# Optimization experiments

Measured on AMD Instinct MI355X. Metric: run time of the kernel, lower is better.

The kernel has to match this reference:

```python
import jax, jax.numpy as jnp
import numpy as np

K = 3
STRIDE = 1
PAD = 1


def _conv2d(x, w, b):
    y = jax.lax.conv_general_dilated(
        x, w, window_strides=(STRIDE, STRIDE),
        padding=[(PAD, PAD), (PAD, PAD)],
        dimension_numbers=("NCHW", "OIHW", "NCHW"))
    return y + b[None, :, None, None]


def _bilinear_sample(xb, py, px):
    # xb: [C, H, W]; py, px: [K2, Ho, Wo] float sample coords
    C, H, W = xb.shape
    y0 = jnp.floor(py)
    x0 = jnp.floor(px)
    ay = py - y0  # frac weights
    ax = px - x0
    out = jnp.zeros((C,) + py.shape, dtype=xb.dtype)
    corners = [
        (y0, x0, (1.0 - ay) * (1.0 - ax)),
        (y0, x0 + 1.0, (1.0 - ay) * ax),
        (y0 + 1.0, x0, ay * (1.0 - ax)),
        (y0 + 1.0, x0 + 1.0, ay * ax),
    ]
    for yc, xc, wgt in corners:
        valid = (yc >= 0) & (yc < H) & (xc >= 0) & (xc < W)
        yi = jnp.clip(yc, 0, H - 1).astype(jnp.int32)
        xi = jnp.clip(xc, 0, W - 1).astype(jnp.int32)
        g = xb[:, yi, xi]  # [C, K2, Ho, Wo]
        out = out + g * (wgt * valid.astype(xb.dtype))[None]
    return out


def _deform_forward(x, weight, bias, p_weight, p_bias):
    B, Cin, H, W = x.shape
    Cout = weight.shape[0]
    K2 = K * K
    # offset / mask prediction conv
    pout = _conv2d(x, p_weight, p_bias)  # [B, 3*K2, Ho, Wo]
    o1, o2, m = jnp.split(pout, 3, axis=1)
    offset = jnp.concatenate([o1, o2], axis=1)  # [B, 2*K2, Ho, Wo]
    mask = jax.nn.sigmoid(m)  # [B, K2, Ho, Wo]
    Ho, Wo = mask.shape[2], mask.shape[3]
    # torchvision layout: channel 2k = dy_k, 2k+1 = dx_k
    off = offset.reshape(B, K2, 2, Ho, Wo)
    dy, dx = off[:, :, 0], off[:, :, 1]  # [B, K2, Ho, Wo]
    ki = (jnp.arange(K2) // K).astype(x.dtype)  # kernel row
    kj = (jnp.arange(K2) % K).astype(x.dtype)   # kernel col
    base_y = jnp.arange(Ho, dtype=x.dtype) * STRIDE - PAD  # [Ho]
    base_x = jnp.arange(Wo, dtype=x.dtype) * STRIDE - PAD  # [Wo]
    py = base_y[None, None, :, None] + ki[None, :, None, None] + dy
    px = base_x[None, None, None, :] + kj[None, :, None, None] + dx
    sampled = jax.vmap(_bilinear_sample)(x, py, px)  # [B, Cin, K2, Ho, Wo]
    sampled = sampled * mask[:, None]
    w = weight.reshape(Cout, Cin, K2)
    out = jnp.einsum('bckhw,ock->bohw', sampled, w) + bias[None, :, None, None]
    return out


def setup_inputs() -> dict:
    key = jax.random.key(0)
    k1, k2, k3 = jax.random.split(key, 3)
    B, Cin, Cout, H, W = 4, 256, 256, 64, 64
    x = jax.random.normal(k1, (B, Cin, H, W), dtype=jnp.float32)
    fan_in = Cin * K * K
    weight = jax.random.normal(k2, (Cout, Cin, K, K), dtype=jnp.float32) / np.sqrt(fan_in)
    bias = jnp.zeros((Cout,), dtype=jnp.float32)
    # small random offset/mask predictor (zero-init in the original; randomized
    # here so the deformable sampling path is exercised)
    p_weight = jax.random.normal(k3, (3 * K * K, Cin, K, K), dtype=jnp.float32) * 0.02
    p_bias = jnp.zeros((3 * K * K,), dtype=jnp.float32)
    return {"x": x, "weight": weight, "bias": bias, "p_weight": p_weight, "p_bias": p_bias}


def reference(x, weight, bias, p_weight, p_bias):
    return _deform_forward(x, weight, bias, p_weight, p_bias)
```

## Files before the change

kernel.cpp:

```cpp
#include <hip/hip_runtime.h>
#include <stdint.h>


#define CIN 256
#define COUT 256
#define HWS 4096
#define MTOT 16384
#define KTOT 2304
#define SPLITK 8

typedef __attribute__((ext_vector_type(8))) short bf16x8;
typedef __attribute__((ext_vector_type(4))) float f32x4;

__device__ __forceinline__ unsigned short f2bf(float f) {
  unsigned int u = __float_as_uint(f);
  unsigned int r = (u + 0x7fffu + ((u >> 16) & 1u)) >> 16;
  return (unsigned short)r;
}
__device__ __forceinline__ float bf2f(unsigned short u) {
  return __uint_as_float(((unsigned int)u) << 16);
}

__device__ __forceinline__ void gload_lds16(const void* g, void* l) {
  __builtin_amdgcn_global_load_lds((const __attribute__((address_space(1))) void*)g,
                                   (__attribute__((address_space(3))) void*)l, 16, 0, 0);
}

__global__ __launch_bounds__(256) void prep_and_transpose(const float* __restrict__ x,
                                                          const float* __restrict__ w,
                                                          const float* __restrict__ pw,
                                                          unsigned short* __restrict__ xt,
                                                          unsigned short* __restrict__ WB,
                                                          unsigned short* __restrict__ PWs,
                                                          unsigned short* __restrict__ zerop) {
  __shared__ float tile[32][33];
  int bid = blockIdx.x;
  if (bid < 4096) {
    int b = bid >> 10;
    int rest = bid & 1023;
    int hw0 = (rest & 127) * 32;
    int c0 = ((rest >> 7) & 7) * 32;
    int tx = threadIdx.x & 31, ty = threadIdx.x >> 5;
    for (int i = ty; i < 32; i += 8)
      tile[i][tx] = x[(size_t)(b * CIN + c0 + i) * HWS + hw0 + tx];
    __syncthreads();
    for (int r = ty; r < 32; r += 8)
      xt[(size_t)(b * HWS + hw0 + r) * CIN + c0 + tx] = f2bf(tile[tx][r]);
  } else {
    int idx = (bid - 4096) * 256 + threadIdx.x;
    if (idx < 512)
      *(uint4*)(zerop + idx * 8) = make_uint4(0, 0, 0, 0);
    if (idx < KTOT * COUT) {
      int f = idx;
      int e = f & 7;
      int row = (f >> 3) & 15;
      int quad = (f >> 7) & 3;
      int j = (f >> 9) & 15;
      int t = f >> 13;
      int kk = t * 32 + quad * 8 + e;
      int o = j * 16 + row;
      int k = kk >> 8, c = kk & 255;
      WB[f] = f2bf(w[o * KTOT + c * 9 + k]);
    } else {
      int f2 = idx - KTOT * COUT;
      int t_ = f2 & 7;
      int rest = f2 >> 3;
      int j = rest & 31;
      int kk = (rest >> 5) * 8 + t_;
      int k = kk >> 8, c = kk & 255;
      float v = (j < 27) ? pw[j * KTOT + c * 9 + k] : 0.0f;
      PWs[f2] = f2bf(v);
    }
  }
}

__global__ __launch_bounds__(256) void offset_conv_sk(const unsigned short* __restrict__ xt,
                                                      const unsigned short* __restrict__ PWs,
                                                      const unsigned short* __restrict__ zerop,
                                                      float* __restrict__ Pbuf) {
  __shared__ unsigned short Al[64 * 32];
  __shared__ unsigned short Bl[1024];
  int tid = threadIdx.x;
  int lane = tid & 63, wv = tid >> 6;
  int mt = (blockIdx.x & 7) * 32 + (blockIdx.x >> 3);
  int m0 = mt * 64;
  int s = blockIdx.y;
  int b = m0 >> 12;
  int hw0 = m0 & 4095;
  f32x4 acc[2] = {};

  for (int tt = 0; tt < 72 / SPLITK; ++tt) {
    int t = s * (72 / SPLITK) + tt;
    int k = t >> 3, c0 = (t & 7) * 32;
    int dyk = k / 3 - 1;
    int dxk = k % 3 - 1;
    __syncthreads();
    if (tid < 128)
      gload_lds16(PWs + (size_t)t * 1024 + tid * 8, &Bl[tid * 8]);
    {
      int r = tid >> 2;
      int hw = hw0 + r;
      int h = hw >> 6, wwp = hw & 63;
      int y = h + dyk, xx = wwp + dxk;
      bool valid = ((unsigned)y < 64u) && ((unsigned)xx < 64u);
      const unsigned short* src = valid
          ? xt + ((size_t)((b << 12) + (y << 6) + xx) << 8) + c0 + (tid & 3) * 8
          : zerop;
      gload_lds16(src, &Al[tid * 8]);
    }
    __syncthreads();
    int row = lane & 15, quad = lane >> 4;
    bf16x8 af = *(const bf16x8*)&Al[(wv * 16 + row) * 32 + quad * 8];
    for (int j = 0; j < 2; ++j) {
      bf16x8 bfr = *(const bf16x8*)&Bl[(quad * 32 + j * 16 + row) * 8];
      acc[j] = __builtin_amdgcn_mfma_f32_16x16x32_bf16(af, bfr, acc[j], 0, 0, 0);
    }
  }

  int row = lane & 15, quad = lane >> 4;
  for (int j = 0; j < 2; ++j) {
    int n = j * 16 + row;
    for (int r_ = 0; r_ < 4; ++r_) {
      int m = m0 + wv * 16 + quad * 4 + r_;
      Pbuf[((size_t)s * MTOT + m) * 32 + n] = acc[j][r_];
    }
  }
}

__global__ __launch_bounds__(256) void sample9(const unsigned short* __restrict__ xt,
                                               const float* __restrict__ Pbuf,
                                               const float* __restrict__ p_bias,
                                               unsigned short* __restrict__ A) {
  __shared__ int4 dI[4][9];
  __shared__ float4 dW[4][9];
  int tid = threadIdx.x;
  int reg = blockIdx.x & 7;
  int mb = reg * 2048 + (blockIdx.x >> 3) * 4;

  if (tid < 36) {
    int lm = tid / 9, k = tid - lm * 9;
    int m = mb + lm;
    float dy = p_bias[2 * k];
    float dx = p_bias[2 * k + 1];
    float mv = p_bias[18 + k];
#pragma unroll
    for (int s = 0; s < SPLITK; ++s) {
      const float* p = Pbuf + ((size_t)s * MTOT + m) * 32;
      dy += p[2 * k];
      dx += p[2 * k + 1];
      mv += p[18 + k];
    }
    float mk = 1.0f / (1.0f + __expf(-mv));

    int hw = m & 4095, h = hw >> 6, ww = hw & 63;
    float py = (float)(h - 1 + k / 3) + dy;
    float px = (float)(ww - 1 + k % 3) + dx;
    float y0f = floorf(py), x0f = floorf(px);
    float ay = py - y0f, ax = px - x0f;
    int y0 = (int)y0f, x0 = (int)x0f;

    float w00 = (1.f - ay) * (1.f - ax) * mk;
    float w01 = (1.f - ay) * ax * mk;
    float w10 = ay * (1.f - ax) * mk;
    float w11 = ay * ax * mk;

    float vy0 = ((unsigned)y0 < 64u) ? 1.f : 0.f;
    float vy1 = ((unsigned)(y0 + 1) < 64u) ? 1.f : 0.f;
    float vx0 = ((unsigned)x0 < 64u) ? 1.f : 0.f;
    float vx1 = ((unsigned)(x0 + 1) < 64u) ? 1.f : 0.f;
    w00 *= vy0 * vx0; w01 *= vy0 * vx1; w10 *= vy1 * vx0; w11 *= vy1 * vx1;

    int yc0 = min(max(y0, 0), 63), yc1 = min(max(y0 + 1, 0), 63);
    int xc0 = min(max(x0, 0), 63), xc1 = min(max(x0 + 1, 0), 63);

    dI[lm][k] = make_int4((yc0 * 64 + xc0) * 256, (yc0 * 64 + xc1) * 256,
                          (yc1 * 64 + xc0) * 256, (yc1 * 64 + xc1) * 256);
    dW[lm][k] = make_float4(w00, w01, w10, w11);
  }
  __syncthreads();

  int wv = tid >> 6, lane = tid & 63;
  int m = mb + wv;
  int b = m >> 12;
  const unsigned short* xtb = xt + (((size_t)b << 12) << 8);
  unsigned short* abase = A + (((size_t)(m >> 4) * 72 + (lane >> 3)) * 16 + (m & 15)) * 32
                            + ((lane >> 1) & 3) * 8 + (lane & 1) * 4;

#pragma unroll
  for (int k = 0; k < 9; ++k) {
    int4 o4 = dI[wv][k];
    float4 w4 = dW[wv][k];
    ushort4 t00 = *(const ushort4*)(xtb + o4.x + 4 * lane);
    ushort4 t01 = *(const ushort4*)(xtb + o4.y + 4 * lane);
    ushort4 t10 = *(const ushort4*)(xtb + o4.z + 4 * lane);
    ushort4 t11 = *(const ushort4*)(xtb + o4.w + 4 * lane);
    float r0 = w4.x * bf2f(t00.x) + w4.y * bf2f(t01.x) + w4.z * bf2f(t10.x) + w4.w * bf2f(t11.x);
    float r1 = w4.x * bf2f(t00.y) + w4.y * bf2f(t01.y) + w4.z * bf2f(t10.y) + w4.w * bf2f(t11.y);
    float r2 = w4.x * bf2f(t00.z) + w4.y * bf2f(t01.z) + w4.z * bf2f(t10.z) + w4.w * bf2f(t11.z);
    float r3 = w4.x * bf2f(t00.w) + w4.y * bf2f(t01.w) + w4.z * bf2f(t10.w) + w4.w * bf2f(t11.w);
    ushort4 o;
    o.x = f2bf(r0); o.y = f2bf(r1); o.z = f2bf(r2); o.w = f2bf(r3);
    *(ushort4*)(abase + (size_t)k * 8 * 512) = o;
  }
}

#define LOADSET(SA0, SA1, SB0, SB1, SB2, SB3, TT)                         \
  {                                                                       \
    const unsigned short* a0_ = ap0 + (size_t)(TT) * 512;                 \
    const unsigned short* a1_ = ap1 + (size_t)(TT) * 512;                 \
    const unsigned short* bt_ = bp + (size_t)(TT) * 8192;                 \
    SA0 = *(const bf16x8*)(a0_);                                          \
    SA1 = *(const bf16x8*)(a1_);                                          \
    SB0 = *(const bf16x8*)(bt_);                                          \
    SB1 = *(const bf16x8*)(bt_ + 512);                                    \
    SB2 = *(const bf16x8*)(bt_ + 1024);                                   \
    SB3 = *(const bf16x8*)(bt_ + 1536);                                   \
  }

#define COMPUTESET(SA0, SA1, SB0, SB1, SB2, SB3)                                        \
  acc[0][0] = __builtin_amdgcn_mfma_f32_16x16x32_bf16(SA0, SB0, acc[0][0], 0, 0, 0);    \
  acc[0][1] = __builtin_amdgcn_mfma_f32_16x16x32_bf16(SA0, SB1, acc[0][1], 0, 0, 0);    \
  acc[0][2] = __builtin_amdgcn_mfma_f32_16x16x32_bf16(SA0, SB2, acc[0][2], 0, 0, 0);    \
  acc[0][3] = __builtin_amdgcn_mfma_f32_16x16x32_bf16(SA0, SB3, acc[0][3], 0, 0, 0);    \
  acc[1][0] = __builtin_amdgcn_mfma_f32_16x16x32_bf16(SA1, SB0, acc[1][0], 0, 0, 0);    \
  acc[1][1] = __builtin_amdgcn_mfma_f32_16x16x32_bf16(SA1, SB1, acc[1][1], 0, 0, 0);    \
  acc[1][2] = __builtin_amdgcn_mfma_f32_16x16x32_bf16(SA1, SB2, acc[1][2], 0, 0, 0);    \
  acc[1][3] = __builtin_amdgcn_mfma_f32_16x16x32_bf16(SA1, SB3, acc[1][3], 0, 0, 0);

__global__ __launch_bounds__(256) void main_gemm(const unsigned short* __restrict__ A2,
                                                 const unsigned short* __restrict__ WB,
                                                 const float* __restrict__ bias,
                                                 float* __restrict__ out) {
  int tid = threadIdx.x;
  int lane = tid & 63, wv = tid >> 6;
  int bid = blockIdx.x;
  int xcd = bid & 7;
  int wgrp = bid >> 3;
  int mt = xcd * 16 + (wgrp >> 2);
  int nb = wgrp & 3;
  int m0 = mt * 128;
  int n0 = nb * 64;
  int wm = wv * 32;
  int row = lane & 15, quad = lane >> 4;
  f32x4 acc[2][4] = {};

  int mb0 = (m0 + wm) >> 4;
  const unsigned short* ap0 = A2 + (size_t)mb0 * 72 * 512 + row * 32 + quad * 8;
  const unsigned short* ap1 = ap0 + (size_t)72 * 512;
  const unsigned short* bp = WB + (size_t)(nb * 4) * 512 + quad * 128 + row * 8;

  bf16x8 s0a0, s0a1, s0b0, s0b1, s0b2, s0b3;
  bf16x8 s1a0, s1a1, s1b0, s1b1, s1b2, s1b3;
  bf16x8 s2a0, s2a1, s2b0, s2b1, s2b2, s2b3;
  bf16x8 s3a0, s3a1, s3b0, s3b1, s3b2, s3b3;

  LOADSET(s0a0, s0a1, s0b0, s0b1, s0b2, s0b3, 0)
  LOADSET(s1a0, s1a1, s1b0, s1b1, s1b2, s1b3, 1)
  LOADSET(s2a0, s2a1, s2b0, s2b1, s2b2, s2b3, 2)
  LOADSET(s3a0, s3a1, s3b0, s3b1, s3b2, s3b3, 3)

#pragma unroll 1
  for (int t = 0; t < 68; t += 4) {
    COMPUTESET(s0a0, s0a1, s0b0, s0b1, s0b2, s0b3)
    LOADSET(s0a0, s0a1, s0b0, s0b1, s0b2, s0b3, t + 4)
    COMPUTESET(s1a0, s1a1, s1b0, s1b1, s1b2, s1b3)
    LOADSET(s1a0, s1a1, s1b0, s1b1, s1b2, s1b3, t + 5)
    COMPUTESET(s2a0, s2a1, s2b0, s2b1, s2b2, s2b3)
    LOADSET(s2a0, s2a1, s2b0, s2b1, s2b2, s2b3, t + 6)
    COMPUTESET(s3a0, s3a1, s3b0, s3b1, s3b2, s3b3)
    LOADSET(s3a0, s3a1, s3b0, s3b1, s3b2, s3b3, t + 7)
  }
  COMPUTESET(s0a0, s0a1, s0b0, s0b1, s0b2, s0b3)
  COMPUTESET(s1a0, s1a1, s1b0, s1b1, s1b2, s1b3)
  COMPUTESET(s2a0, s2a1, s2b0, s2b1, s2b2, s2b3)
  COMPUTESET(s3a0, s3a1, s3b0, s3b1, s3b2, s3b3)

  int b = m0 >> 12, hw0 = m0 & 4095;
#pragma unroll
  for (int j = 0; j < 4; ++j) {
    int o = n0 + j * 16 + row;
    float bo = bias[o];
#pragma unroll
    for (int i = 0; i < 2; ++i) {
      int hw = hw0 + wm + i * 16 + quad * 4;
      float4 v;
      v.x = acc[i][j][0] + bo;
      v.y = acc[i][j][1] + bo;
      v.z = acc[i][j][2] + bo;
      v.w = acc[i][j][3] + bo;
      *(float4*)(out + (((size_t)(b * COUT + o)) << 12) + hw) = v;
    }
  }
}

extern "C" void kernel_launch(void* const* d_in, const int* in_sizes, int n_in,
                              void* d_out, int out_size, void* d_ws, size_t ws_size,
                              hipStream_t stream) {
  const float* x        = (const float*)d_in[0];
  const float* weight   = (const float*)d_in[1];
  const float* bias     = (const float*)d_in[2];
  const float* p_weight = (const float*)d_in[3];
  const float* p_bias   = (const float*)d_in[4];
  float* out = (float*)d_out;
  char* ws = (char*)d_ws;

  const size_t OFF_XT   = 0;
  const size_t OFF_WB   = OFF_XT + 8388608;
  const size_t OFF_PW   = OFF_WB + 1179648;
  const size_t OFF_P    = OFF_PW + 147456;
  const size_t OFF_ZP   = OFF_P + 16777216;
  const size_t OFF_A    = OFF_ZP + 8192;

  unsigned short* xt    = (unsigned short*)(ws + OFF_XT);
  unsigned short* WB    = (unsigned short*)(ws + OFF_WB);
  unsigned short* PWs   = (unsigned short*)(ws + OFF_PW);
  float* Pbuf           = (float*)(ws + OFF_P);
  unsigned short* zerop = (unsigned short*)(ws + OFF_ZP);
  unsigned short* Amat  = (unsigned short*)(ws + OFF_A);

  prep_and_transpose<<<4096 + 2592, 256, 0, stream>>>(x, weight, p_weight, xt, WB, PWs, zerop);
  offset_conv_sk<<<dim3(MTOT / 64, SPLITK), 256, 0, stream>>>(xt, PWs, zerop, Pbuf);
  sample9<<<MTOT / 4, 256, 0, stream>>>(xt, Pbuf, p_bias, Amat);
  main_gemm<<<512, 256, 0, stream>>>(Amat, WB, bias, out);
}
```

Measured before the change: 150.9 us.

## Fuse bilinear sampling into main GEMM, replacing materialized im2col matrix with index table

The sampling kernel that wrote a bf16 im2col matrix to global memory is split: a small kernel now precomputes per-(pixel, tap) corner offsets and weights. The GEMM kernel then gathers the four corners, interpolates into double-buffered LDS A tiles, and runs MFMA on them while prefetching the next K-slice. This removes the write and re-read of the large sampled matrix. In exchange the GEMM uses 64x256 tiles with only 256 blocks, a barrier every K step, and gather latency inside the main loop.

```diff
diff --git a/kernel.cpp b/kernel.cpp
--- a/kernel.cpp
+++ b/kernel.cpp
@@ -127,162 +127,183 @@
   }
 }
 
-__global__ __launch_bounds__(256) void sample9(const unsigned short* __restrict__ xt,
-                                               const float* __restrict__ Pbuf,
-                                               const float* __restrict__ p_bias,
-                                               unsigned short* __restrict__ A) {
-  __shared__ int4 dI[4][9];
-  __shared__ float4 dW[4][9];
-  int tid = threadIdx.x;
-  int reg = blockIdx.x & 7;
-  int mb = reg * 2048 + (blockIdx.x >> 3) * 4;
-
-  if (tid < 36) {
-    int lm = tid / 9, k = tid - lm * 9;
-    int m = mb + lm;
-    float dy = p_bias[2 * k];
-    float dx = p_bias[2 * k + 1];
-    float mv = p_bias[18 + k];
+__global__ __launch_bounds__(256) void index_prep(const float* __restrict__ Pbuf,
+                                                  const float* __restrict__ p_bias,
+                                                  int4* __restrict__ DIW) {
+  int gid = blockIdx.x * 256 + threadIdx.x;
+  int m = gid / 9;
+  int k = gid - m * 9;
+
+  float dy = p_bias[2 * k];
+  float dx = p_bias[2 * k + 1];
+  float mv = p_bias[18 + k];
 #pragma unroll
-    for (int s = 0; s < SPLITK; ++s) {
-      const float* p = Pbuf + ((size_t)s * MTOT + m) * 32;
-      dy += p[2 * k];
-      dx += p[2 * k + 1];
-      mv += p[18 + k];
-    }
-    float mk = 1.0f / (1.0f + __expf(-mv));
-
-    int hw = m & 4095, h = hw >> 6, ww = hw & 63;
-    float py = (float)(h - 1 + k / 3) + dy;
-    float px = (float)(ww - 1 + k % 3) + dx;
-    float y0f = floorf(py), x0f = floorf(px);
-    float ay = py - y0f, ax = px - x0f;
-    int y0 = (int)y0f, x0 = (int)x0f;
-
-    float w00 = (1.f - ay) * (1.f - ax) * mk;
-    float w01 = (1.f - ay) * ax * mk;
-    float w10 = ay * (1.f - ax) * mk;
-    float w11 = ay * ax * mk;
-
-    float vy0 = ((unsigned)y0 < 64u) ? 1.f : 0.f;
-    float vy1 = ((unsigned)(y0 + 1) < 64u) ? 1.f : 0.f;
-    float vx0 = ((unsigned)x0 < 64u) ? 1.f : 0.f;
-    float vx1 = ((unsigned)(x0 + 1) < 64u) ? 1.f : 0.f;
-    w00 *= vy0 * vx0; w01 *= vy0 * vx1; w10 *= vy1 * vx0; w11 *= vy1 * vx1;
-
-    int yc0 = min(max(y0, 0), 63), yc1 = min(max(y0 + 1, 0), 63);
-    int xc0 = min(max(x0, 0), 63), xc1 = min(max(x0 + 1, 0), 63);
-
-    dI[lm][k] = make_int4((yc0 * 64 + xc0) * 256, (yc0 * 64 + xc1) * 256,
-                          (yc1 * 64 + xc0) * 256, (yc1 * 64 + xc1) * 256);
-    dW[lm][k] = make_float4(w00, w01, w10, w11);
-  }
-  __syncthreads();
-
-  int wv = tid >> 6, lane = tid & 63;
-  int m = mb + wv;
-  int b = m >> 12;
-  const unsigned short* xtb = xt + (((size_t)b << 12) << 8);
-  unsigned short* abase = A + (((size_t)(m >> 4) * 72 + (lane >> 3)) * 16 + (m & 15)) * 32
-                            + ((lane >> 1) & 3) * 8 + (lane & 1) * 4;
-
+  for (int s = 0; s < SPLITK; ++s) {
+    const float* p = Pbuf + ((size_t)s * MTOT + m) * 32;
+    dy += p[2 * k];
+    dx += p[2 * k + 1];
+    mv += p[18 + k];
+  }
+  float mk = 1.0f / (1.0f + __expf(-mv));
+
+  int hw = m & 4095, h = hw >> 6, ww = hw & 63;
+  float py = (float)(h - 1 + k / 3) + dy;
+  float px = (float)(ww - 1 + k % 3) + dx;
+  float y0f = floorf(py), x0f = floorf(px);
+  float ay = py - y0f, ax = px - x0f;
+  int y0 = (int)y0f, x0 = (int)x0f;
+
+  float w00 = (1.f - ay) * (1.f - ax) * mk;
+  float w01 = (1.f - ay) * ax * mk;
+  float w10 = ay * (1.f - ax) * mk;
+  float w11 = ay * ax * mk;
+
+  float vy0 = ((unsigned)y0 < 64u) ? 1.f : 0.f;
+  float vy1 = ((unsigned)(y0 + 1) < 64u) ? 1.f : 0.f;
+  float vx0 = ((unsigned)x0 < 64u) ? 1.f : 0.f;
+  float vx1 = ((unsigned)(x0 + 1) < 64u) ? 1.f : 0.f;
+  w00 *= vy0 * vx0; w01 *= vy0 * vx1; w10 *= vy1 * vx0; w11 *= vy1 * vx1;
+
+  int yc0 = min(max(y0, 0), 63), yc1 = min(max(y0 + 1, 0), 63);
+  int xc0 = min(max(x0, 0), 63), xc1 = min(max(x0 + 1, 0), 63);
+
+  DIW[(size_t)gid * 2] = make_int4((yc0 * 64 + xc0) * 256, (yc0 * 64 + xc1) * 256,
+                                   (yc1 * 64 + xc0) * 256, (yc1 * 64 + xc1) * 256);
+  float4 w4 = make_float4(w00, w01, w10, w11);
+  ((float4*)DIW)[(size_t)gid * 2 + 1] = w4;
+}
+
+__device__ __forceinline__ void bilin8(const bf16x8 g00, const bf16x8 g01,
+                                       const bf16x8 g10, const bf16x8 g11,
+                                       const float4 w4, unsigned short* dst) {
+  bf16x8 o8;
 #pragma unroll
-  for (int k = 0; k < 9; ++k) {
-    int4 o4 = dI[wv][k];
-    float4 w4 = dW[wv][k];
-    ushort4 t00 = *(const ushort4*)(xtb + o4.x + 4 * lane);
-    ushort4 t01 = *(const ushort4*)(xtb + o4.y + 4 * lane);
-    ushort4 t10 = *(const ushort4*)(xtb + o4.z + 4 * lane);
-    ushort4 t11 = *(const ushort4*)(xtb + o4.w + 4 * lane);
-    float r0 = w4.x * bf2f(t00.x) + w4.y * bf2f(t01.x) + w4.z * bf2f(t10.x) + w4.w * bf2f(t11.x);
-    float r1 = w4.x * bf2f(t00.y) + w4.y * bf2f(t01.y) + w4.z * bf2f(t10.y) + w4.w * bf2f(t11.y);
-    float r2 = w4.x * bf2f(t00.z) + w4.y * bf2f(t01.z) + w4.z * bf2f(t10.z) + w4.w * bf2f(t11.z);
-    float r3 = w4.x * bf2f(t00.w) + w4.y * bf2f(t01.w) + w4.z * bf2f(t10.w) + w4.w * bf2f(t11.w);
-    ushort4 o;
-    o.x = f2bf(r0); o.y = f2bf(r1); o.z = f2bf(r2); o.w = f2bf(r3);
-    *(ushort4*)(abase + (size_t)k * 8 * 512) = o;
-  }
-}
-
-#define LOADSET(SA0, SA1, SB0, SB1, SB2, SB3, TT)                         \
-  {                                                                       \
-    const unsigned short* a0_ = ap0 + (size_t)(TT) * 512;                 \
-    const unsigned short* a1_ = ap1 + (size_t)(TT) * 512;                 \
-    const unsigned short* bt_ = bp + (size_t)(TT) * 8192;                 \
-    SA0 = *(const bf16x8*)(a0_);                                          \
-    SA1 = *(const bf16x8*)(a1_);                                          \
-    SB0 = *(const bf16x8*)(bt_);                                          \
-    SB1 = *(const bf16x8*)(bt_ + 512);                                    \
-    SB2 = *(const bf16x8*)(bt_ + 1024);                                   \
-    SB3 = *(const bf16x8*)(bt_ + 1536);                                   \
-  }
-
-#define COMPUTESET(SA0, SA1, SB0, SB1, SB2, SB3)                                        \
-  acc[0][0] = __builtin_amdgcn_mfma_f32_16x16x32_bf16(SA0, SB0, acc[0][0], 0, 0, 0);    \
-  acc[0][1] = __builtin_amdgcn_mfma_f32_16x16x32_bf16(SA0, SB1, acc[0][1], 0, 0, 0);    \
-  acc[0][2] = __builtin_amdgcn_mfma_f32_16x16x32_bf16(SA0, SB2, acc[0][2], 0, 0, 0);    \
-  acc[0][3] = __builtin_amdgcn_mfma_f32_16x16x32_bf16(SA0, SB3, acc[0][3], 0, 0, 0);    \
-  acc[1][0] = __builtin_amdgcn_mfma_f32_16x16x32_bf16(SA1, SB0, acc[1][0], 0, 0, 0);    \
-  acc[1][1] = __builtin_amdgcn_mfma_f32_16x16x32_bf16(SA1, SB1, acc[1][1], 0, 0, 0);    \
-  acc[1][2] = __builtin_amdgcn_mfma_f32_16x16x32_bf16(SA1, SB2, acc[1][2], 0, 0, 0);    \
-  acc[1][3] = __builtin_amdgcn_mfma_f32_16x16x32_bf16(SA1, SB3, acc[1][3], 0, 0, 0);
-
-__global__ __launch_bounds__(256) void main_gemm(const unsigned short* __restrict__ A2,
-                                                 const unsigned short* __restrict__ WB,
-                                                 const float* __restrict__ bias,
-                                                 float* __restrict__ out) {
+  for (int e = 0; e < 8; ++e) {
+    float v = w4.x * bf2f((unsigned short)g00[e]) + w4.y * bf2f((unsigned short)g01[e]) +
+              w4.z * bf2f((unsigned short)g10[e]) + w4.w * bf2f((unsigned short)g11[e]);
+    o8[e] = (short)f2bf(v);
+  }
+  *(bf16x8*)dst = o8;
+}
+
+#define MFMA16(A0, A1, A2_, A3, B0, B1, B2, B3)                                          \
+  acc[0][0] = __builtin_amdgcn_mfma_f32_16x16x32_bf16(A0, B0, acc[0][0], 0, 0, 0);       \
+  acc[0][1] = __builtin_amdgcn_mfma_f32_16x16x32_bf16(A0, B1, acc[0][1], 0, 0, 0);       \
+  acc[0][2] = __builtin_amdgcn_mfma_f32_16x16x32_bf16(A0, B2, acc[0][2], 0, 0, 0);       \
+  acc[0][3] = __builtin_amdgcn_mfma_f32_16x16x32_bf16(A0, B3, acc[0][3], 0, 0, 0);       \
+  acc[1][0] = __builtin_amdgcn_mfma_f32_16x16x32_bf16(A1, B0, acc[1][0], 0, 0, 0);       \
+  acc[1][1] = __builtin_amdgcn_mfma_f32_16x16x32_bf16(A1, B1, acc[1][1], 0, 0, 0);       \
+  acc[1][2] = __builtin_amdgcn_mfma_f32_16x16x32_bf16(A1, B2, acc[1][2], 0, 0, 0);       \
+  acc[1][3] = __builtin_amdgcn_mfma_f32_16x16x32_bf16(A1, B3, acc[1][3], 0, 0, 0);       \
+  acc[2][0] = __builtin_amdgcn_mfma_f32_16x16x32_bf16(A2_, B0, acc[2][0], 0, 0, 0);      \
+  acc[2][1] = __builtin_amdgcn_mfma_f32_16x16x32_bf16(A2_, B1, acc[2][1], 0, 0, 0);      \
+  acc[2][2] = __builtin_amdgcn_mfma_f32_16x16x32_bf16(A2_, B2, acc[2][2], 0, 0, 0);      \
+  acc[2][3] = __builtin_amdgcn_mfma_f32_16x16x32_bf16(A2_, B3, acc[2][3], 0, 0, 0);      \
+  acc[3][0] = __builtin_amdgcn_mfma_f32_16x16x32_bf16(A3, B0, acc[3][0], 0, 0, 0);       \
+  acc[3][1] = __builtin_amdgcn_mfma_f32_16x16x32_bf16(A3, B1, acc[3][1], 0, 0, 0);       \
+  acc[3][2] = __builtin_amdgcn_mfma_f32_16x16x32_bf16(A3, B2, acc[3][2], 0, 0, 0);       \
+  acc[3][3] = __builtin_amdgcn_mfma_f32_16x16x32_bf16(A3, B3, acc[3][3], 0, 0, 0);
+
+#define FITER(T, PAR, BC0, BC1, BC2, BC3, BN0, BN1, BN2, BN3)                            \
+  {                                                                                      \
+    if ((T) <= 69) {                                                                     \
+      if ((((T) + 2) & 7) == 0) dI4 = Tbl[r][((T) + 2) >> 3][0];                         \
+      int cq = (((T) + 2) & 7) * 32 + qo;                                                \
+      g00 = *(const bf16x8*)(xtb + dI4.x + cq);                                          \
+      g01 = *(const bf16x8*)(xtb + dI4.y + cq);                                          \
+      g10 = *(const bf16x8*)(xtb + dI4.z + cq);                                          \
+      g11 = *(const bf16x8*)(xtb + dI4.w + cq);                                          \
+    }                                                                                    \
+    if ((T) <= 70) {                                                                     \
+      const unsigned short* bt_ = bpb + (size_t)((T) + 1) * 8192;                        \
+      BN0 = *(const bf16x8*)(bt_);                                                       \
+      BN1 = *(const bf16x8*)(bt_ + 512);                                                 \
+      BN2 = *(const bf16x8*)(bt_ + 1024);                                                \
+      BN3 = *(const bf16x8*)(bt_ + 1536);                                                \
+    }                                                                                    \
+    afr0 = *(const bf16x8*)&As[PAR][row][quad * 8];                                      \
+    afr1 = *(const bf16x8*)&As[PAR][16 + row][quad * 8];                                 \
+    afr2 = *(const bf16x8*)&As[PAR][32 + row][quad * 8];                                 \
+    afr3 = *(const bf16x8*)&As[PAR][48 + row][quad * 8];                                 \
+    if ((T) <= 70) {                                                                     \
+      if ((((T) + 1) & 7) == 0) dW4 = *(float4*)&Tbl[r][((T) + 1) >> 3][1];              \
+      bilin8(gp0, gp1, gp2, gp3, dW4, &As[PAR ^ 1][r][qo]);                              \
+    }                                                                                    \
+    MFMA16(afr0, afr1, afr2, afr3, BC0, BC1, BC2, BC3)                                   \
+    __syncthreads();                                                                     \
+  }
+
+__global__ __launch_bounds__(256, 1) void fused_gemm(const unsigned short* __restrict__ xt,
+                                                     const int4* __restrict__ DIW,
+                                                     const unsigned short* __restrict__ WB,
+                                                     const float* __restrict__ bias,
+                                                     float* __restrict__ out) {
+  __shared__ unsigned short As[2][64][40];
+  __shared__ int4 Tbl[64][9][2];
+
   int tid = threadIdx.x;
   int lane = tid & 63, wv = tid >> 6;
-  int bid = blockIdx.x;
-  int xcd = bid & 7;
-  int wgrp = bid >> 3;
-  int mt = xcd * 16 + (wgrp >> 2);
-  int nb = wgrp & 3;
-  int m0 = mt * 128;
-  int n0 = nb * 64;
-  int wm = wv * 32;
+  int mt = (blockIdx.x & 7) * 32 + (blockIdx.x >> 3);
+  int mb = mt * 64;
+  int b = mb >> 12;
+  int hw0 = mb & 4095;
+  const unsigned short* xtb = xt + ((size_t)b << 20);
+
+  {
+    const int4* src = DIW + (size_t)mb * 18;
+    int4* dst = (int4*)Tbl;
+    for (int i = tid; i < 1152; i += 256)
+      gload_lds16(src + i, dst + i);
+  }
+  __syncthreads();
+
+  int r = tid >> 2;
+  int qo = (tid & 3) * 8;
+
+  int4 dI4 = Tbl[r][0][0];
+  float4 dW4 = *(float4*)&Tbl[r][0][1];
+
   int row = lane & 15, quad = lane >> 4;
-  f32x4 acc[2][4] = {};
-
-  int mb0 = (m0 + wm) >> 4;
-  const unsigned short* ap0 = A2 + (size_t)mb0 * 72 * 512 + row * 32 + quad * 8;
-  const unsigned short* ap1 = ap0 + (size_t)72 * 512;
-  const unsigned short* bp = WB + (size_t)(nb * 4) * 512 + quad * 128 + row * 8;
-
-  bf16x8 s0a0, s0a1, s0b0, s0b1, s0b2, s0b3;
-  bf16x8 s1a0, s1a1, s1b0, s1b1, s1b2, s1b3;
-  bf16x8 s2a0, s2a1, s2b0, s2b1, s2b2, s2b3;
-  bf16x8 s3a0, s3a1, s3b0, s3b1, s3b2, s3b3;
-
-  LOADSET(s0a0, s0a1, s0b0, s0b1, s0b2, s0b3, 0)
-  LOADSET(s1a0, s1a1, s1b0, s1b1, s1b2, s1b3, 1)
-  LOADSET(s2a0, s2a1, s2b0, s2b1, s2b2, s2b3, 2)
-  LOADSET(s3a0, s3a1, s3b0, s3b1, s3b2, s3b3, 3)
+  const unsigned short* bpb = WB + (size_t)wv * 4 * 512 + quad * 128 + row * 8;
+
+  f32x4 acc[4][4] = {};
+  bf16x8 g00, g01, g10, g11;
+  bf16x8 gp0, gp1, gp2, gp3;
+  bf16x8 bA0, bA1, bA2, bA3, bB0, bB1, bB2, bB3;
+  bf16x8 afr0, afr1, afr2, afr3;
+
+  {
+    g00 = *(const bf16x8*)(xtb + dI4.x + qo);
+    g01 = *(const bf16x8*)(xtb + dI4.y + qo);
+    g10 = *(const bf16x8*)(xtb + dI4.z + qo);
+    g11 = *(const bf16x8*)(xtb + dI4.w + qo);
+    bA0 = *(const bf16x8*)(bpb);
+    bA1 = *(const bf16x8*)(bpb + 512);
+    bA2 = *(const bf16x8*)(bpb + 1024);
+    bA3 = *(const bf16x8*)(bpb + 1536);
+    bilin8(g00, g01, g10, g11, dW4, &As[0][r][qo]);
+    g00 = *(const bf16x8*)(xtb + dI4.x + 32 + qo);
+    g01 = *(const bf16x8*)(xtb + dI4.y + 32 + qo);
+    g10 = *(const bf16x8*)(xtb + dI4.z + 32 + qo);
+    g11 = *(const bf16x8*)(xtb + dI4.w + 32 + qo);
+  }
+  __syncthreads();
 
 #pragma unroll 1
-  for (int t = 0; t < 68; t += 4) {
-    COMPUTESET(s0a0, s0a1, s0b0, s0b1, s0b2, s0b3)
-    LOADSET(s0a0, s0a1, s0b0, s0b1, s0b2, s0b3, t + 4)
-    COMPUTESET(s1a0, s1a1, s1b0, s1b1, s1b2, s1b3)
-    LOADSET(s1a0, s1a1, s1b0, s1b1, s1b2, s1b3, t + 5)
-    COMPUTESET(s2a0, s2a1, s2b0, s2b1, s2b2, s2b3)
-    LOADSET(s2a0, s2a1, s2b0, s2b1, s2b2, s2b3, t + 6)
-    COMPUTESET(s3a0, s3a1, s3b0, s3b1, s3b2, s3b3)
-    LOADSET(s3a0, s3a1, s3b0, s3b1, s3b2, s3b3, t + 7)
-  }
-  COMPUTESET(s0a0, s0a1, s0b0, s0b1, s0b2, s0b3)
-  COMPUTESET(s1a0, s1a1, s1b0, s1b1, s1b2, s1b3)
-  COMPUTESET(s2a0, s2a1, s2b0, s2b1, s2b2, s2b3)
-  COMPUTESET(s3a0, s3a1, s3b0, s3b1, s3b2, s3b3)
-
-  int b = m0 >> 12, hw0 = m0 & 4095;
+  for (int t = 0; t < 72; t += 2) {
+    gp0 = g00; gp1 = g01; gp2 = g10; gp3 = g11;
+    FITER(t, 0, bA0, bA1, bA2, bA3, bB0, bB1, bB2, bB3)
+    gp0 = g00; gp1 = g01; gp2 = g10; gp3 = g11;
+    FITER(t + 1, 1, bB0, bB1, bB2, bB3, bA0, bA1, bA2, bA3)
+  }
+
 #pragma unroll
   for (int j = 0; j < 4; ++j) {
-    int o = n0 + j * 16 + row;
+    int o = wv * 64 + j * 16 + row;
     float bo = bias[o];
 #pragma unroll
-    for (int i = 0; i < 2; ++i) {
-      int hw = hw0 + wm + i * 16 + quad * 4;
+    for (int i = 0; i < 4; ++i) {
+      int hw = hw0 + i * 16 + quad * 4;
       float4 v;
       v.x = acc[i][j][0] + bo;
       v.y = acc[i][j][1] + bo;
@@ -309,17 +330,17 @@
   const size_t OFF_PW   = OFF_WB + 1179648;
   const size_t OFF_P    = OFF_PW + 147456;
   const size_t OFF_ZP   = OFF_P + 16777216;
-  const size_t OFF_A    = OFF_ZP + 8192;
+  const size_t OFF_DIW  = OFF_ZP + 8192;
 
   unsigned short* xt    = (unsigned short*)(ws + OFF_XT);
   unsigned short* WB    = (unsigned short*)(ws + OFF_WB);
   unsigned short* PWs   = (unsigned short*)(ws + OFF_PW);
   float* Pbuf           = (float*)(ws + OFF_P);
   unsigned short* zerop = (unsigned short*)(ws + OFF_ZP);
-  unsigned short* Amat  = (unsigned short*)(ws + OFF_A);
+  int4* DIW             = (int4*)(ws + OFF_DIW);
 
   prep_and_transpose<<<4096 + 2592, 256, 0, stream>>>(x, weight, p_weight, xt, WB, PWs, zerop);
   offset_conv_sk<<<dim3(MTOT / 64, SPLITK), 256, 0, stream>>>(xt, PWs, zerop, Pbuf);
-  sample9<<<MTOT / 4, 256, 0, stream>>>(xt, Pbuf, p_bias, Amat);
-  main_gemm<<<512, 256, 0, stream>>>(Amat, WB, bias, out);
-}
+  index_prep<<<576, 256, 0, stream>>>(Pbuf, p_bias, DIW);
+  fused_gemm<<<256, 256, 0, stream>>>(xt, DIW, WB, bias, out);
+}
```

Measured after the change: 141.9 us. 1.06x faster.
